# Performance work log

Hardware: AMD Instinct MI355X
Metric: run time of the kernel (lower is better)

Reference implementation:

```python
import jax, jax.numpy as jnp
import numpy as np

# Mamba3TextEncoder config (class .small() defaults)
B_SZ, SEQ = 4, 512
VOCAB, D_MODEL, N_LAYERS = 32000, 768, 12
N_STATE, EXPAND, HEADDIM, NGROUPS, EMBED = 64, 2, 32, 1, 1536
D_INNER = EXPAND * D_MODEL            # 1536
NHEADS = D_INNER // HEADDIM           # 48
CONV_DIM = D_INNER + 2 * NGROUPS * N_STATE  # 1664 (x, B, C go through depthwise conv)
K_CONV = 4
PROJ_IN = 2 * D_INNER + 2 * NGROUPS * N_STATE + NHEADS  # z, xBC, dt


def setup_inputs() -> dict:
    key = jax.random.key(0)
    ks = jax.random.split(key, 16)
    s = 0.02
    return {
        "token_ids": jax.random.randint(ks[0], (B_SZ, SEQ), 0, VOCAB),
        "embed_W": jax.random.normal(ks[1], (VOCAB, D_MODEL), jnp.float32) * s,
        "ln_W": jnp.ones((N_LAYERS, D_MODEL), jnp.float32),
        "in_proj_W": jax.random.normal(ks[2], (N_LAYERS, D_MODEL, PROJ_IN), jnp.float32) * s,
        "conv_W": jax.random.normal(ks[3], (N_LAYERS, CONV_DIM, 1, K_CONV), jnp.float32) * 0.1,
        "conv_b": jnp.zeros((N_LAYERS, CONV_DIM), jnp.float32),
        "dt_bias": jax.random.uniform(ks[4], (N_LAYERS, NHEADS), jnp.float32, -4.6, -2.0),
        "A_log": jnp.tile(jnp.log(jnp.arange(1, NHEADS + 1, dtype=jnp.float32))[None], (N_LAYERS, 1)),
        "D": jnp.ones((N_LAYERS, NHEADS), jnp.float32),
        "norm_W": jnp.ones((N_LAYERS, D_INNER), jnp.float32),
        "out_proj_W": jax.random.normal(ks[5], (N_LAYERS, D_INNER, D_MODEL), jnp.float32) * s,
        "final_norm_W": jnp.ones((D_MODEL,), jnp.float32),
        "proj_W": jax.random.normal(ks[6], (D_MODEL, EMBED), jnp.float32) * s,
        "proj_b": jnp.zeros((EMBED,), jnp.float32),
    }


def _rmsnorm(x, w, eps=1e-5):
    return x * jax.lax.rsqrt(jnp.mean(x * x, axis=-1, keepdims=True) + eps) * w


def _causal_conv(x, w, b):
    # x: [B,S,C] depthwise causal conv, kernel K_CONV
    y = jax.lax.conv_general_dilated(
        x.transpose(0, 2, 1), w, (1,), [(K_CONV - 1, 0)],
        dimension_numbers=("NCH", "OIH", "NCH"), feature_group_count=CONV_DIM)
    return y.transpose(0, 2, 1) + b


def _ssm(xs, dt, A, Bm, Cm):
    # selective scan. xs:[B,S,H,P] dt:[B,S,H] A:[H] Bm,Cm:[B,S,N] (ngroups=1)
    decay = jnp.exp(dt * A)              # [B,S,H]
    dtx = dt[..., None] * xs             # [B,S,H,P]
    h0 = jnp.zeros((xs.shape[0], NHEADS, HEADDIM, N_STATE), xs.dtype)

    def step(h, inp):
        dec, dx, b, c = inp              # [B,H],[B,H,P],[B,N],[B,N]
        h = dec[..., None, None] * h + dx[..., None] * b[:, None, None, :]
        y = jnp.einsum("bhpn,bn->bhp", h, c)
        return h, y

    inputs = (decay.transpose(1, 0, 2), dtx.transpose(1, 0, 2, 3),
              Bm.transpose(1, 0, 2), Cm.transpose(1, 0, 2))
    _, ys = jax.lax.scan(step, h0, inputs)
    return ys.transpose(1, 0, 2, 3)      # [B,S,H,P]


def reference(token_ids, embed_W, ln_W, in_proj_W, conv_W, conv_b, dt_bias,
              A_log, D, norm_W, out_proj_W, final_norm_W, proj_W, proj_b):
    x = embed_W[token_ids]                               # [B,S,D]
    for l in range(N_LAYERS):
        h = _rmsnorm(x, ln_W[l])
        zxbcdt = h @ in_proj_W[l]                        # [B,S,PROJ_IN]
        z = zxbcdt[..., :D_INNER]
        xBC = zxbcdt[..., D_INNER:D_INNER + CONV_DIM]
        dt_raw = zxbcdt[..., D_INNER + CONV_DIM:]        # [B,S,H]
        xBC = jax.nn.silu(_causal_conv(xBC, conv_W[l], conv_b[l]))
        xs = xBC[..., :D_INNER].reshape(*xBC.shape[:2], NHEADS, HEADDIM)
        Bm = xBC[..., D_INNER:D_INNER + N_STATE]
        Cm = xBC[..., D_INNER + N_STATE:]
        dt = jax.nn.softplus(dt_raw + dt_bias[l])
        A = -jnp.exp(A_log[l])
        y = _ssm(xs, dt, A, Bm, Cm) + D[l][None, None, :, None] * xs
        y = y.reshape(*y.shape[:2], D_INNER)
        y = _rmsnorm(y * jax.nn.silu(z), norm_W[l])      # gated RMSNorm
        x = x + y @ out_proj_W[l]
    x = _rmsnorm(x, final_norm_W)
    pooled = x.mean(axis=1)                              # [B,D]
    proj = pooled @ proj_W + proj_b                      # [B,EMBED]
    n = jnp.sqrt(jnp.sum(proj * proj, axis=-1, keepdims=True))
    return proj / jnp.maximum(n, 1e-12)
```

## Files before the change

kernel.cpp:

```cpp
#include <hip/hip_runtime.h>
#include <math.h>

typedef __bf16 bf16x8 __attribute__((ext_vector_type(8)));
typedef short  s16x8  __attribute__((ext_vector_type(8)));
typedef float  f32x4  __attribute__((ext_vector_type(4)));

static constexpr int BSZ = 4, SEQ = 512, DM = 768;
static constexpr int DIN = 1536, NH = 48, HP = 32, NS = 64;
static constexpr int CDIM = 1664;
static constexpr int PROJ_IN = 3248;
static constexpr int LDZX = 3328;
static constexpr int ROWS = BSZ * SEQ;
static constexpr int EMBED = 1536;
static constexpr int NLAYERS = 12;

using gptr_t = const __attribute__((address_space(1))) void*;
using lptr_t = __attribute__((address_space(3))) void*;

__device__ __forceinline__ unsigned short f2bf(float f) {
  unsigned u = __builtin_bit_cast(unsigned, f);
  u += 0x7FFF + ((u >> 16) & 1);
  return (unsigned short)(u >> 16);
}
__device__ __forceinline__ float bf2f(unsigned short u) {
  unsigned v = (unsigned)u << 16;
  return __builtin_bit_cast(float, v);
}
__device__ __forceinline__ float sigm(float x) { return 1.f / (1.f + __expf(-x)); }
__device__ __forceinline__ float sp(float x) { return (x > 15.f) ? x : log1pf(__expf(x)); }

__device__ __forceinline__ void gll16(const void* g, void* l) {
  __builtin_amdgcn_global_load_lds((gptr_t)g, (lptr_t)l, 16, 0, 0);
}
__device__ __forceinline__ f32x4 mfma16(s16x8 a, s16x8 b, f32x4 c) {
  return __builtin_amdgcn_mfma_f32_16x16x32_bf16(
      __builtin_bit_cast(bf16x8, a), __builtin_bit_cast(bf16x8, b), c, 0, 0, 0);
}

template <int NW>
__device__ __forceinline__ float block_sum(float v) {
#pragma unroll
  for (int o = 32; o; o >>= 1) v += __shfl_xor(v, o);
  __shared__ float red[NW];
  if ((threadIdx.x & 63) == 0) red[threadIdx.x >> 6] = v;
  __syncthreads();
  float s = red[0];
#pragma unroll
  for (int i = 1; i < NW; ++i) s += red[i];
  return s;
}

__global__ void embed_k(const int* __restrict__ tok, const float* __restrict__ eW,
                        float* __restrict__ x, unsigned short* __restrict__ x16,
                        float* __restrict__ ssq1p) {
  int bt = blockIdx.x, tid = threadIdx.x;
  float4 v = ((const float4*)(eW + (size_t)tok[bt] * DM))[tid];
  ((float4*)(x + (size_t)bt * DM))[tid] = v;
  unsigned long long pk =
      (unsigned long long)f2bf(v.x) | ((unsigned long long)f2bf(v.y) << 16) |
      ((unsigned long long)f2bf(v.z) << 32) | ((unsigned long long)f2bf(v.w) << 48);
  *(unsigned long long*)(x16 + (size_t)bt * DM + tid * 4) = pk;
  float ss = v.x * v.x + v.y * v.y + v.z * v.z + v.w * v.w;
  float tot = block_sum<3>(ss);
  if (tid < 24) ssq1p[(size_t)bt * 24 + tid] = (tid == 0) ? tot : 0.f;
}

__global__ void transpose_cvt(const float* __restrict__ W, const float* __restrict__ sc,
                              unsigned short* __restrict__ Wt, int K, int N, int Npad) {
  __shared__ float tile[32][68];
  int l = blockIdx.z;
  const float* Wl = W + (size_t)l * K * N;
  const float* scl = sc + (size_t)l * K;
  unsigned short* Wtl = Wt + (size_t)l * Npad * K;
  int nb = blockIdx.x * 64, kb = blockIdx.y * 32;
  int tid = threadIdx.x;
#pragma unroll
  for (int rep = 0; rep < 2; ++rep) {
    int f = rep * 256 + tid;
    int k = f >> 4, c4 = f & 15;
    int n = nb + c4 * 4;
    float s = scl[kb + k];
    float4 v = {0.f, 0.f, 0.f, 0.f};
    if (n + 3 < N) {
      v = *(const float4*)(Wl + (size_t)(kb + k) * N + n);
    } else if (n < N) {
      float t_[4] = {0.f, 0.f, 0.f, 0.f};
      for (int j = 0; j < 4; ++j) if (n + j < N) t_[j] = Wl[(size_t)(kb + k) * N + n + j];
      v = {t_[0], t_[1], t_[2], t_[3]};
    }
    tile[k][c4 * 4 + 0] = v.x * s; tile[k][c4 * 4 + 1] = v.y * s;
    tile[k][c4 * 4 + 2] = v.z * s; tile[k][c4 * 4 + 3] = v.w * s;
  }
  __syncthreads();
#pragma unroll
  for (int rep = 0; rep < 2; ++rep) {
    int f = rep * 256 + tid;
    int n = f >> 3, k8 = f & 7;
    unsigned long long pk =
        (unsigned long long)f2bf(tile[k8 * 4 + 0][n]) |
        ((unsigned long long)f2bf(tile[k8 * 4 + 1][n]) << 16) |
        ((unsigned long long)f2bf(tile[k8 * 4 + 2][n]) << 32) |
        ((unsigned long long)f2bf(tile[k8 * 4 + 3][n]) << 48);
    *(unsigned long long*)(Wtl + (size_t)(nb + n) * K + kb + k8 * 4) = pk;
  }
}

template <int BM, int BN, int MODE>
__global__ __launch_bounds__(256) void gemm_k(
    const unsigned short* __restrict__ A, const unsigned short* __restrict__ Bt,
    int K, const float* __restrict__ ssqp, void* __restrict__ O0,
    void* __restrict__ O1, void* __restrict__ O2,
    unsigned short* __restrict__ x16o, float* __restrict__ ssqo) {
  constexpr int AIT = BM / 32, BIT = BN / 32, NST = AIT + BIT;
  constexpr int FM = BM / 32, FN = BN / 32;
  constexpr int NSSQ = (MODE == 0) ? 24 : 48;
  constexpr float INVD = (MODE == 0) ? (1.f / 768.f) : (1.f / 1536.f);
  __shared__ unsigned short lA[2][BM * 64], lB[2][BN * 64];
  __shared__ float rss[BM];
  int tid = threadIdx.x, lane = tid & 63, wv = tid >> 6;
  int flat = blockIdx.y * gridDim.x + blockIdx.x;
  int q8 = (gridDim.x * gridDim.y) >> 3;
  int nf = (flat & 7) * q8 + (flat >> 3);
  int bx = nf % gridDim.x, by = nf / gridDim.x;
  int m0 = by * BM, n0 = bx * BN;
  int wm = (wv >> 1) * (BM / 2), wn = (wv & 1) * (BN / 2);
  int NK = K >> 6;
  auto stage = [&](int kt, int buf) {
#pragma unroll
    for (int i = 0; i < AIT; ++i) {
      int flt = i * 256 + tid, rr = flt >> 3, cc = flt & 7;
      gll16(A + (size_t)(m0 + rr) * K + kt + (cc ^ (rr & 7)) * 8, (char*)lA[buf] + flt * 16);
    }
#pragma unroll
    for (int i = 0; i < BIT; ++i) {
      int flt = i * 256 + tid, rr = flt >> 3, cc = flt & 7;
      gll16(Bt + (size_t)(n0 + rr) * K + kt + (cc ^ (rr & 7)) * 8, (char*)lB[buf] + flt * 16);
    }
  };
  stage(0, 0);
  if (tid < BM) {
    const float* p = ssqp + (size_t)(m0 + tid) * NSSQ;
    float s = 0.f;
#pragma unroll
    for (int j = 0; j < NSSQ; ++j) s += p[j];
    rss[tid] = rsqrtf(s * INVD + 1e-5f);
  }
  __syncthreads();
  f32x4 acc[FM][FN] = {};
  for (int i = 0; i < NK; ++i) {
    if (i + 1 < NK) {
      stage((i + 1) << 6, (i + 1) & 1);
      asm volatile("s_waitcnt vmcnt(%0)" :: "i"(NST) : "memory");
    } else {
      asm volatile("s_waitcnt vmcnt(0)" ::: "memory");
    }
    __builtin_amdgcn_s_barrier();
    __builtin_amdgcn_sched_barrier(0);
    const unsigned short* cA = lA[i & 1];
    const unsigned short* cB = lB[i & 1];
#pragma unroll
    for (int ks = 0; ks < 2; ++ks) {
      s16x8 a[FM], b[FN];
#pragma unroll
      for (int mi = 0; mi < FM; ++mi) {
        int row = wm + mi * 16 + (lane & 15);
        int ch = (ks * 4 + (lane >> 4)) ^ (row & 7);
        a[mi] = *(const s16x8*)((const char*)cA + row * 128 + ch * 16);
      }
#pragma unroll
      for (int nj = 0; nj < FN; ++nj) {
        int row = wn + nj * 16 + (lane & 15);
        int ch = (ks * 4 + (lane >> 4)) ^ (row & 7);
        b[nj] = *(const s16x8*)((const char*)cB + row * 128 + ch * 16);
      }
#pragma unroll
      for (int mi = 0; mi < FM; ++mi)
#pragma unroll
        for (int nj = 0; nj < FN; ++nj)
          acc[mi][nj] = mfma16(a[mi], b[nj], acc[mi][nj]);
    }
    __builtin_amdgcn_s_barrier();
  }
#pragma unroll
  for (int mi = 0; mi < FM; ++mi) {
    int rl0 = wm + mi * 16 + ((lane >> 4) << 2);
    float rsr[4];
#pragma unroll
    for (int rg = 0; rg < 4; ++rg) rsr[rg] = rss[rl0 + rg];
    float part[4] = {0.f, 0.f, 0.f, 0.f};
#pragma unroll
    for (int nj = 0; nj < FN; ++nj) {
      int col = n0 + wn + nj * 16 + (lane & 15);
#pragma unroll
      for (int rg = 0; rg < 4; ++rg) {
        int row = m0 + rl0 + rg;
        float vv = acc[mi][nj][rg] * rsr[rg];
        if constexpr (MODE == 0) {
          if (n0 < DIN) {
            ((unsigned short*)O0)[(size_t)row * DIN + col] = f2bf(vv);
          } else if (n0 < DIN + CDIM) {
            ((float*)O1)[(size_t)row * CDIM + (col - DIN)] = vv;
          } else {
            int c2 = col - (DIN + CDIM);
            if (c2 < NH) ((float*)O2)[(size_t)row * NH + c2] = vv;
          }
        } else {
          size_t idx = (size_t)row * DM + col;
          float xn = vv + ((float*)O0)[idx];
          ((float*)O0)[idx] = xn;
          x16o[idx] = f2bf(xn);
          part[rg] += xn * xn;
        }
      }
    }
    if constexpr (MODE == 1) {
#pragma unroll
      for (int rg = 0; rg < 4; ++rg) {
#pragma unroll
        for (int off = 1; off < 16; off <<= 1) part[rg] += __shfl_xor(part[rg], off);
      }
      if ((lane & 15) == 0) {
#pragma unroll
        for (int rg = 0; rg < 4; ++rg)
          ssqo[(size_t)(m0 + rl0 + rg) * 24 + bx * 2 + (wn >> 5)] = part[rg];
      }
    }
  }
}

__global__ __launch_bounds__(256) void conv_dt_k(
    const float* __restrict__ xbc, const float* __restrict__ cw, const float* __restrict__ cb,
    const float* __restrict__ dtraw, const float* __restrict__ dbias,
    unsigned short* __restrict__ xs16, unsigned short* __restrict__ dtxT,
    unsigned short* __restrict__ Bbf, unsigned short* __restrict__ Cbf,
    float* __restrict__ dts) {
  __shared__ float stg[11][256];
  __shared__ float dtl[8][48];
  int tid = threadIdx.x;
  int chunk = blockIdx.x;
  int bt0 = blockIdx.y * 8;
  int t0 = bt0 & (SEQ - 1);
  int cbase = chunk * 256;
  for (int f = tid; f < 11 * 64; f += 256) {
    int row = f >> 6, c4 = f & 63;
    int s = t0 - 3 + row;
    int col = cbase + c4 * 4;
    float4 v = {0.f, 0.f, 0.f, 0.f};
    if (s >= 0 && col + 3 < CDIM) {
      v = *(const float4*)(xbc + (size_t)(bt0 - 3 + row) * CDIM + col);
    }
    *(float4*)&stg[row][c4 * 4] = v;
  }
  if (chunk < 6) {
    for (int idx = tid; idx < 384; idx += 256) {
      int r = idx / 48, hh = idx - r * 48;
      dtl[r][hh] = sp(dtraw[(size_t)(bt0 + r) * NH + hh] + dbias[hh]);
    }
  }
  __syncthreads();
  int c = cbase + tid;
  if (chunk < 6) {
    float w0 = cw[c * 4], w1 = cw[c * 4 + 1], w2 = cw[c * 4 + 2], w3 = cw[c * 4 + 3];
    float bias = cb[c];
    int hh = c >> 5, p = c & 31, b = bt0 >> 9;
    s16x8 pk;
#pragma unroll
    for (int r = 0; r < 8; ++r) {
      float a = bias + stg[r][tid] * w0 + stg[r + 1][tid] * w1 + stg[r + 2][tid] * w2 +
                stg[r + 3][tid] * w3;
      float sv = a * sigm(a);
      xs16[(size_t)(bt0 + r) * DIN + c] = f2bf(sv);
      pk[r] = (short)f2bf(sv * dtl[r][hh]);
    }
    *reinterpret_cast<s16x8*>(dtxT + ((((size_t)b * NH + hh) * HP + p) * SEQ + t0)) = pk;
  } else if (tid < 128) {
    int cc = DIN + tid;
    float w0 = cw[cc * 4], w1 = cw[cc * 4 + 1], w2 = cw[cc * 4 + 2], w3 = cw[cc * 4 + 3];
    float bias = cb[cc];
#pragma unroll
    for (int r = 0; r < 8; ++r) {
      float a = bias + stg[r][tid] * w0 + stg[r + 1][tid] * w1 + stg[r + 2][tid] * w2 +
                stg[r + 3][tid] * w3;
      float sv = a * sigm(a);
      if (tid < 64) Bbf[(size_t)(bt0 + r) * NS + tid] = f2bf(sv);
      else          Cbf[(size_t)(bt0 + r) * NS + (tid - 64)] = f2bf(sv);
    }
  } else if (tid < 176) {
    int hh = tid - 128;
    float bias_ = dbias[hh];
    float v[8];
#pragma unroll
    for (int r = 0; r < 8; ++r) v[r] = sp(dtraw[(size_t)(bt0 + r) * NH + hh] + bias_);
    float4 a4 = {v[0], v[1], v[2], v[3]}, b4 = {v[4], v[5], v[6], v[7]};
    float* dp = dts + ((size_t)(bt0 >> 9) * NH + hh) * SEQ + t0;
    *(float4*)dp = a4;
    *(float4*)(dp + 4) = b4;
  }
}

__global__ __launch_bounds__(256) void scan_k(
    const unsigned short* __restrict__ Bbf, const unsigned short* __restrict__ Cbf,
    const unsigned short* __restrict__ dtxT, const unsigned short* __restrict__ xs16,
    const float* __restrict__ dts, const unsigned short* __restrict__ zb,
    const float* __restrict__ alog, const float* __restrict__ Dvec,
    unsigned short* __restrict__ g16, float* __restrict__ ssq2p) {
  __shared__ unsigned short CbPt[64 * 64];
  __shared__ unsigned short Bb[2][64 * 64], Dx[2][32 * 64];
  __shared__ float lsb[SEQ];
  __shared__ float wtot[4];
  __shared__ int sfirst;
  int tid = threadIdx.x, lane = tid & 63, wv = tid >> 6;
  int tb = blockIdx.x, h = blockIdx.y, b = blockIdx.z;
  int t0 = tb * 64;
  const unsigned short* dxrow = dtxT + ((size_t)b * NH + h) * HP * SEQ;

#pragma unroll
  for (int i = 0; i < 2; ++i) {
    int flt = i * 256 + tid, rr = flt >> 3, cc = flt & 7;
    gll16(Cbf + (size_t)(b * SEQ + t0 + rr) * NS + (cc ^ (rr & 7)) * 8, (char*)CbPt + flt * 16);
  }
  float Ah = -__expf(alog[h]);
  int t2 = tid * 2;
  float2 dv = *(const float2*)(dts + ((size_t)b * NH + h) * SEQ + t2);
  float d0 = dv.x * Ah, d1 = dv.y * Ah;
  float ps = d0 + d1;
  float v = ps;
#pragma unroll
  for (int off = 1; off < 64; off <<= 1) {
    float u = __shfl_up(v, off);
    if (lane >= off) v += u;
  }
  if (lane == 63) wtot[wv] = v;
  if (tid == 0) sfirst = tb;
  __syncthreads();
  float wpre = 0.f;
#pragma unroll
  for (int w = 0; w < 3; ++w) wpre += (w < wv) ? wtot[w] : 0.f;
  float excl = v + wpre - ps;
  lsb[t2] = excl + d0;
  lsb[t2 + 1] = excl + d0 + d1;
  __syncthreads();
  float REF = lsb[t0];
  if (tid < tb && (REF - lsb[tid * 64 + 63] >= -12.f)) atomicMin(&sfirst, tid);
  __syncthreads();
  int st0 = sfirst;

#pragma unroll
  for (int i = 0; i < 2; ++i) {
    int flt = i * 256 + tid, rr = flt >> 3, cc = flt & 7;
    gll16(Bbf + (size_t)(b * SEQ + st0 * 64 + rr) * NS + (cc ^ (rr & 7)) * 8,
          (char*)Bb[st0 & 1] + flt * 16);
  }
  { int rr = tid >> 3, cc = tid & 7;
    gll16(dxrow + (size_t)rr * SEQ + st0 * 64 + (cc ^ (rr & 7)) * 8,
          (char*)Dx[st0 & 1] + tid * 16); }

  float lt[4], elt[4];
  int trb = wv * 16 + ((lane >> 4) << 2);
#pragma unroll
  for (int rg = 0; rg < 4; ++rg) {
    lt[rg] = lsb[t0 + trb + rg];
    elt[rg] = __expf(lt[rg] - REF);
  }
  s16x8 aC[2];
  f32x4 yacc[2] = {};

  for (int st = st0; st <= tb; ++st) {
    int s0 = st * 64;
    if (st < tb) {
      int s1 = s0 + 64;
#pragma unroll
      for (int i = 0; i < 2; ++i) {
        int flt = i * 256 + tid, rr = flt >> 3, cc = flt & 7;
        gll16(Bbf + (size_t)(b * SEQ + s1 + rr) * NS + (cc ^ (rr & 7)) * 8,
              (char*)Bb[(st + 1) & 1] + flt * 16);
      }
      { int rr = tid >> 3, cc = tid & 7;
        gll16(dxrow + (size_t)rr * SEQ + s1 + (cc ^ (rr & 7)) * 8,
              (char*)Dx[(st + 1) & 1] + tid * 16); }
      asm volatile("s_waitcnt vmcnt(3)" ::: "memory");
    } else {
      asm volatile("s_waitcnt vmcnt(0)" ::: "memory");
    }
    __builtin_amdgcn_s_barrier();
    __builtin_amdgcn_sched_barrier(0);
    const unsigned short* Bcur = Bb[st & 1];
    const unsigned short* Dcur = Dx[st & 1];
    if (st == st0) {
#pragma unroll
      for (int ks = 0; ks < 2; ++ks) {
        int row = wv * 16 + (lane & 15);
        int ch = (ks * 4 + (lane >> 4)) ^ (row & 7);
        aC[ks] = *(const s16x8*)((const char*)CbPt + row * 128 + ch * 16);
      }
    }
    float lsv[4];
#pragma unroll
    for (int sq = 0; sq < 4; ++sq) lsv[sq] = lsb[s0 + sq * 16 + (lane & 15)];
    f32x4 gf[4] = {};
    __builtin_amdgcn_s_setprio(1);
#pragma unroll
    for (int sq = 0; sq < 4; ++sq)
#pragma unroll
      for (int ks = 0; ks < 2; ++ks) {
        int row = sq * 16 + (lane & 15);
        int ch = (ks * 4 + (lane >> 4)) ^ (row & 7);
        s16x8 bB = *(const s16x8*)((const char*)Bcur + row * 128 + ch * 16);
        gf[sq] = mfma16(aC[ks], bB, gf[sq]);
      }
    __builtin_amdgcn_s_setprio(0);
    if (st < tb) {
      float es[4];
#pragma unroll
      for (int sq = 0; sq < 4; ++sq) es[sq] = __expf(REF - lsv[sq]);
#pragma unroll
      for (int sq = 0; sq < 4; ++sq) {
        int scol = sq * 16 + (lane & 15);
#pragma unroll
        for (int rg = 0; rg < 4; ++rg) {
          int trow = trb + rg;
          int off = (trow * 128 + scol * 2) ^ ((trow & 7) << 4);
          *(unsigned short*)((char*)CbPt + off) = f2bf(gf[sq][rg] * (elt[rg] * es[sq]));
        }
      }
    } else {
#pragma unroll
      for (int sq = 0; sq < 4; ++sq) {
        int scol = sq * 16 + (lane & 15);
        int sg = s0 + scol;
#pragma unroll
        for (int rg = 0; rg < 4; ++rg) {
          int trow = trb + rg, tg = t0 + trow;
          float wgt = (sg <= tg) ? __expf(lt[rg] - lsv[sq]) : 0.f;
          int off = (trow * 128 + scol * 2) ^ ((trow & 7) << 4);
          *(unsigned short*)((char*)CbPt + off) = f2bf(gf[sq][rg] * wgt);
        }
      }
    }
    __builtin_amdgcn_s_setprio(1);
#pragma unroll
    for (int ks = 0; ks < 2; ++ks) {
      int row = wv * 16 + (lane & 15);
      int ch = (ks * 4 + (lane >> 4)) ^ (row & 7);
      s16x8 aP = *(const s16x8*)((const char*)CbPt + row * 128 + ch * 16);
#pragma unroll
      for (int pq = 0; pq < 2; ++pq) {
        int prow = pq * 16 + (lane & 15);
        int pch = (ks * 4 + (lane >> 4)) ^ (prow & 7);
        s16x8 bD = *(const s16x8*)((const char*)Dcur + prow * 128 + pch * 16);
        yacc[pq] = mfma16(aP, bD, yacc[pq]);
      }
    }
    __builtin_amdgcn_s_setprio(0);
    __builtin_amdgcn_s_barrier();
  }
  float Dh = Dvec[h];
  float part[4] = {0.f, 0.f, 0.f, 0.f};
#pragma unroll
  for (int pq = 0; pq < 2; ++pq) {
#pragma unroll
    for (int rg = 0; rg < 4; ++rg) {
      int trow = trb + rg;
      int tg = t0 + trow;
      int p = pq * 16 + (lane & 15);
      size_t gi = (size_t)(b * SEQ + tg) * DIN + h * HP + p;
      float xv = bf2f(xs16[gi]);
      float yv = yacc[pq][rg] + Dh * xv;
      float zf = bf2f(zb[gi]);
      float g = yv * zf * sigm(zf);
      g16[gi] = f2bf(g);
      part[rg] += g * g;
    }
  }
#pragma unroll
  for (int rg = 0; rg < 4; ++rg) {
#pragma unroll
    for (int off = 1; off < 16; off <<= 1) part[rg] += __shfl_xor(part[rg], off);
  }
  if ((lane & 15) == 0) {
#pragma unroll
    for (int rg = 0; rg < 4; ++rg)
      ssq2p[(size_t)(b * SEQ + t0 + trb + rg) * 48 + h] = part[rg];
  }
}

__global__ void pool_part_k(const float* __restrict__ x, const float* __restrict__ ssq1p,
                            float* __restrict__ pp) {
  __shared__ float rsl[64];
  int b = blockIdx.y, tc = blockIdx.z, d0 = blockIdx.x * 256, tid = threadIdx.x;
  int t0 = tc * 64;
  if (tid < 64) {
    const float* p = ssq1p + (size_t)(b * SEQ + t0 + tid) * 24;
    float s = 0.f;
#pragma unroll
    for (int j = 0; j < 24; ++j) s += p[j];
    rsl[tid] = rsqrtf(s * (1.f / DM) + 1e-5f);
  }
  __syncthreads();
  int d = d0 + tid;
  float s = 0.f;
#pragma unroll 4
  for (int i = 0; i < 64; ++i) s += x[(size_t)(b * SEQ + t0 + i) * DM + d] * rsl[i];
  pp[((size_t)b * 8 + tc) * DM + d] = s;
}
__global__ void proj_k(const float* __restrict__ pp, const float* __restrict__ fnW,
                       const float* __restrict__ pW, const float* __restrict__ pb,
                       float* __restrict__ ptmp) {
  __shared__ float pl[DM];
  __shared__ float red[4][64];
  int e0 = blockIdx.x * 64, b = blockIdx.y, tid = threadIdx.x;
  for (int i = tid; i < DM; i += 256) {
    float s = 0.f;
#pragma unroll
    for (int c = 0; c < 8; ++c) s += pp[((size_t)b * 8 + c) * DM + i];
    pl[i] = s * (1.f / SEQ) * fnW[i];
  }
  __syncthreads();
  int el = tid & 63, g = tid >> 6;
  int e = e0 + el;
  float s = 0.f;
  for (int d = g * 192; d < (g + 1) * 192; ++d)
    s += pl[d] * pW[(size_t)d * EMBED + e];
  red[g][el] = s;
  __syncthreads();
  if (g == 0) ptmp[b * EMBED + e] = red[0][el] + red[1][el] + red[2][el] + red[3][el] + pb[e];
}
__global__ void l2_k(const float* __restrict__ ptmp, float* __restrict__ out) {
  int b = blockIdx.x;
  float v[6], ss = 0.f;
#pragma unroll
  for (int i = 0; i < 6; ++i) {
    v[i] = ptmp[(size_t)b * EMBED + threadIdx.x + i * 256];
    ss += v[i] * v[i];
  }
  float tot = block_sum<4>(ss);
  float inv = 1.f / fmaxf(sqrtf(tot), 1e-12f);
#pragma unroll
  for (int i = 0; i < 6; ++i)
    out[(size_t)b * EMBED + threadIdx.x + i * 256] = v[i] * inv;
}

extern "C" void kernel_launch(void* const* d_in, const int* in_sizes, int n_in,
                              void* d_out, int out_size, void* d_ws, size_t ws_size,
                              hipStream_t stream) {
  const int*   tok  = (const int*)d_in[0];
  const float* embW = (const float*)d_in[1];
  const float* lnW  = (const float*)d_in[2];
  const float* ipW  = (const float*)d_in[3];
  const float* cW   = (const float*)d_in[4];
  const float* cB   = (const float*)d_in[5];
  const float* dtB  = (const float*)d_in[6];
  const float* Alog = (const float*)d_in[7];
  const float* Dv   = (const float*)d_in[8];
  const float* nW   = (const float*)d_in[9];
  const float* opW  = (const float*)d_in[10];
  const float* fnW  = (const float*)d_in[11];
  const float* pW   = (const float*)d_in[12];
  const float* pb   = (const float*)d_in[13];
  float* out = (float*)d_out;

  char* wsp = (char*)d_ws;
  auto alloc = [&](size_t bytes) {
    char* p = wsp;
    wsp += (bytes + 255) & ~(size_t)255;
    return p;
  };
  float* x      = (float*)alloc((size_t)ROWS * DM * 4);
  float* xbc    = (float*)alloc((size_t)ROWS * CDIM * 4);
  float* dtraw  = (float*)alloc((size_t)ROWS * NH * 4);
  float* dts    = (float*)alloc((size_t)BSZ * NH * SEQ * 4);
  float* ssq1p  = (float*)alloc((size_t)ROWS * 24 * 4);
  float* ssq2p  = (float*)alloc((size_t)ROWS * 48 * 4);
  float* pp     = (float*)alloc((size_t)BSZ * 8 * DM * 4);
  float* ptmp   = (float*)alloc((size_t)BSZ * EMBED * 4);
  unsigned short* x16   = (unsigned short*)alloc((size_t)ROWS * DM * 2);
  unsigned short* zb    = (unsigned short*)alloc((size_t)ROWS * DIN * 2);
  unsigned short* xs16  = (unsigned short*)alloc((size_t)ROWS * DIN * 2);
  unsigned short* g16   = (unsigned short*)alloc((size_t)ROWS * DIN * 2);
  unsigned short* dtxT  = (unsigned short*)alloc((size_t)BSZ * NH * HP * SEQ * 2);
  unsigned short* Bbf   = (unsigned short*)alloc((size_t)ROWS * NS * 2);
  unsigned short* Cbf   = (unsigned short*)alloc((size_t)ROWS * NS * 2);
  unsigned short* wtA   = (unsigned short*)alloc((size_t)NLAYERS * LDZX * DM * 2);
  unsigned short* wtO   = (unsigned short*)alloc((size_t)NLAYERS * DM * DIN * 2);

  embed_k<<<ROWS, 192, 0, stream>>>(tok, embW, x, x16, ssq1p);
  transpose_cvt<<<dim3(LDZX / 64, DM / 32, NLAYERS), 256, 0, stream>>>(
      ipW, lnW, wtA, DM, PROJ_IN, LDZX);
  transpose_cvt<<<dim3(DM / 64, DIN / 32, NLAYERS), 256, 0, stream>>>(
      opW, nW, wtO, DIN, DM, DM);

  for (int l = 0; l < NLAYERS; ++l) {
    gemm_k<128, 64, 0><<<dim3(LDZX / 64, ROWS / 128), 256, 0, stream>>>(
        x16, wtA + (size_t)l * LDZX * DM, DM, ssq1p, zb, xbc, dtraw, nullptr, nullptr);
    conv_dt_k<<<dim3(7, ROWS / 8), 256, 0, stream>>>(
        xbc, cW + (size_t)l * CDIM * 4, cB + (size_t)l * CDIM, dtraw, dtB + l * NH,
        xs16, dtxT, Bbf, Cbf, dts);
    scan_k<<<dim3(SEQ / 64, NH, BSZ), 256, 0, stream>>>(
        Bbf, Cbf, dtxT, xs16, dts, zb, Alog + l * NH, Dv + l * NH, g16, ssq2p);
    gemm_k<64, 64, 1><<<dim3(DM / 64, ROWS / 64), 256, 0, stream>>>(
        g16, wtO + (size_t)l * DM * DIN, DIN, ssq2p, x, nullptr, nullptr, x16, ssq1p);
  }

  pool_part_k<<<dim3(DM / 256, BSZ, 8), 256, 0, stream>>>(x, ssq1p, pp);
  proj_k<<<dim3(EMBED / 64, BSZ), 256, 0, stream>>>(pp, fnW, pW, pb, ptmp);
  l2_k<<<BSZ, 256, 0, stream>>>(ptmp, out);
}
```

Before: 921.9 us.

## Process 128-row output tiles per scan block with 512 threads

The chunked scan kernel now has each block handle 128 time steps (8 waves) instead of 64, so each B and dt·x source chunk loaded into shared memory feeds two 64-row output tiles. The grid halves along the sequence axis and the prefix-sum of decay is computed with one element per thread. The aim is to cut redundant global loads and per-block setup, at the cost of fewer blocks, more LDS per block, and per-wave waitcnt handling. The diagonal masking now covers the last two source chunks for all rows, which lets the upper tile use masked weights even on the earlier chunk.

```diff
diff --git a/kernel.cpp b/kernel.cpp
--- a/kernel.cpp
+++ b/kernel.cpp
@@ -298,87 +298,83 @@
   }
 }
 
-__global__ __launch_bounds__(256) void scan_k(
+__global__ __launch_bounds__(512) void scan_k(
     const unsigned short* __restrict__ Bbf, const unsigned short* __restrict__ Cbf,
     const unsigned short* __restrict__ dtxT, const unsigned short* __restrict__ xs16,
     const float* __restrict__ dts, const unsigned short* __restrict__ zb,
     const float* __restrict__ alog, const float* __restrict__ Dvec,
     unsigned short* __restrict__ g16, float* __restrict__ ssq2p) {
-  __shared__ unsigned short CbPt[64 * 64];
+  __shared__ unsigned short CbPt[128 * 64];
   __shared__ unsigned short Bb[2][64 * 64], Dx[2][32 * 64];
   __shared__ float lsb[SEQ];
-  __shared__ float wtot[4];
+  __shared__ float wtot[8];
   __shared__ int sfirst;
   int tid = threadIdx.x, lane = tid & 63, wv = tid >> 6;
-  int tb = blockIdx.x, h = blockIdx.y, b = blockIdx.z;
-  int t0 = tb * 64;
+  int tb2 = blockIdx.x;
+  int h = blockIdx.y, b = blockIdx.z;
+  int T0 = tb2 * 128;
+  int ST_LAST = 2 * tb2 + 1;
   const unsigned short* dxrow = dtxT + ((size_t)b * NH + h) * HP * SEQ;
 
 #pragma unroll
   for (int i = 0; i < 2; ++i) {
-    int flt = i * 256 + tid, rr = flt >> 3, cc = flt & 7;
-    gll16(Cbf + (size_t)(b * SEQ + t0 + rr) * NS + (cc ^ (rr & 7)) * 8, (char*)CbPt + flt * 16);
+    int flt = i * 512 + tid, rr = flt >> 3, cc = flt & 7;
+    gll16(Cbf + (size_t)(b * SEQ + T0 + rr) * NS + (cc ^ (rr & 7)) * 8, (char*)CbPt + flt * 16);
   }
   float Ah = -__expf(alog[h]);
-  int t2 = tid * 2;
-  float2 dv = *(const float2*)(dts + ((size_t)b * NH + h) * SEQ + t2);
-  float d0 = dv.x * Ah, d1 = dv.y * Ah;
-  float ps = d0 + d1;
-  float v = ps;
+  float d = dts[((size_t)b * NH + h) * SEQ + tid] * Ah;
+  float v = d;
 #pragma unroll
   for (int off = 1; off < 64; off <<= 1) {
     float u = __shfl_up(v, off);
     if (lane >= off) v += u;
   }
   if (lane == 63) wtot[wv] = v;
-  if (tid == 0) sfirst = tb;
+  if (tid == 0) sfirst = 2 * tb2;
   __syncthreads();
   float wpre = 0.f;
 #pragma unroll
-  for (int w = 0; w < 3; ++w) wpre += (w < wv) ? wtot[w] : 0.f;
-  float excl = v + wpre - ps;
-  lsb[t2] = excl + d0;
-  lsb[t2 + 1] = excl + d0 + d1;
-  __syncthreads();
-  float REF = lsb[t0];
-  if (tid < tb && (REF - lsb[tid * 64 + 63] >= -12.f)) atomicMin(&sfirst, tid);
+  for (int w = 0; w < 7; ++w) wpre += (w < wv) ? wtot[w] : 0.f;
+  lsb[tid] = v + wpre;
+  __syncthreads();
+  float REF = lsb[T0];
+  if (tid < 2 * tb2 && (REF - lsb[tid * 64 + 63] >= -12.f)) atomicMin(&sfirst, tid);
   __syncthreads();
   int st0 = sfirst;
 
-#pragma unroll
-  for (int i = 0; i < 2; ++i) {
-    int flt = i * 256 + tid, rr = flt >> 3, cc = flt & 7;
+  { int rr = tid >> 3, cc = tid & 7;
     gll16(Bbf + (size_t)(b * SEQ + st0 * 64 + rr) * NS + (cc ^ (rr & 7)) * 8,
-          (char*)Bb[st0 & 1] + flt * 16);
-  }
-  { int rr = tid >> 3, cc = tid & 7;
+          (char*)Bb[st0 & 1] + tid * 16); }
+  if (tid < 256) {
+    int rr = tid >> 3, cc = tid & 7;
     gll16(dxrow + (size_t)rr * SEQ + st0 * 64 + (cc ^ (rr & 7)) * 8,
-          (char*)Dx[st0 & 1] + tid * 16); }
+          (char*)Dx[st0 & 1] + tid * 16);
+  }
 
   float lt[4], elt[4];
   int trb = wv * 16 + ((lane >> 4) << 2);
 #pragma unroll
   for (int rg = 0; rg < 4; ++rg) {
-    lt[rg] = lsb[t0 + trb + rg];
+    lt[rg] = lsb[T0 + trb + rg];
     elt[rg] = __expf(lt[rg] - REF);
   }
   s16x8 aC[2];
   f32x4 yacc[2] = {};
 
-  for (int st = st0; st <= tb; ++st) {
+  for (int st = st0; st <= ST_LAST; ++st) {
     int s0 = st * 64;
-    if (st < tb) {
+    if (st < ST_LAST) {
       int s1 = s0 + 64;
-#pragma unroll
-      for (int i = 0; i < 2; ++i) {
-        int flt = i * 256 + tid, rr = flt >> 3, cc = flt & 7;
+      { int rr = tid >> 3, cc = tid & 7;
         gll16(Bbf + (size_t)(b * SEQ + s1 + rr) * NS + (cc ^ (rr & 7)) * 8,
-              (char*)Bb[(st + 1) & 1] + flt * 16);
-      }
-      { int rr = tid >> 3, cc = tid & 7;
+              (char*)Bb[(st + 1) & 1] + tid * 16); }
+      if (tid < 256) {
+        int rr = tid >> 3, cc = tid & 7;
         gll16(dxrow + (size_t)rr * SEQ + s1 + (cc ^ (rr & 7)) * 8,
-              (char*)Dx[(st + 1) & 1] + tid * 16); }
-      asm volatile("s_waitcnt vmcnt(3)" ::: "memory");
+              (char*)Dx[(st + 1) & 1] + tid * 16);
+      }
+      if (wv < 4) { asm volatile("s_waitcnt vmcnt(2)" ::: "memory"); }
+      else        { asm volatile("s_waitcnt vmcnt(1)" ::: "memory"); }
     } else {
       asm volatile("s_waitcnt vmcnt(0)" ::: "memory");
     }
@@ -409,7 +405,7 @@
         gf[sq] = mfma16(aC[ks], bB, gf[sq]);
       }
     __builtin_amdgcn_s_setprio(0);
-    if (st < tb) {
+    if (st < ST_LAST - 1) {
       float es[4];
 #pragma unroll
       for (int sq = 0; sq < 4; ++sq) es[sq] = __expf(REF - lsv[sq]);
@@ -430,7 +426,7 @@
         int sg = s0 + scol;
 #pragma unroll
         for (int rg = 0; rg < 4; ++rg) {
-          int trow = trb + rg, tg = t0 + trow;
+          int trow = trb + rg, tg = T0 + trow;
           float wgt = (sg <= tg) ? __expf(lt[rg] - lsv[sq]) : 0.f;
           int off = (trow * 128 + scol * 2) ^ ((trow & 7) << 4);
           *(unsigned short*)((char*)CbPt + off) = f2bf(gf[sq][rg] * wgt);
@@ -461,7 +457,7 @@
 #pragma unroll
     for (int rg = 0; rg < 4; ++rg) {
       int trow = trb + rg;
-      int tg = t0 + trow;
+      int tg = T0 + trow;
       int p = pq * 16 + (lane & 15);
       size_t gi = (size_t)(b * SEQ + tg) * DIN + h * HP + p;
       float xv = bf2f(xs16[gi]);
@@ -480,7 +476,7 @@
   if ((lane & 15) == 0) {
 #pragma unroll
     for (int rg = 0; rg < 4; ++rg)
-      ssq2p[(size_t)(b * SEQ + t0 + trb + rg) * 48 + h] = part[rg];
+      ssq2p[(size_t)(b * SEQ + T0 + trb + rg) * 48 + h] = part[rg];
   }
 }
 
@@ -595,7 +591,7 @@
     conv_dt_k<<<dim3(7, ROWS / 8), 256, 0, stream>>>(
         xbc, cW + (size_t)l * CDIM * 4, cB + (size_t)l * CDIM, dtraw, dtB + l * NH,
         xs16, dtxT, Bbf, Cbf, dts);
-    scan_k<<<dim3(SEQ / 64, NH, BSZ), 256, 0, stream>>>(
+    scan_k<<<dim3(SEQ / 128, NH, BSZ), 512, 0, stream>>>(
         Bbf, Cbf, dtxT, xs16, dts, zb, Alog + l * NH, Dv + l * NH, g16, ssq2p);
     gemm_k<64, 64, 1><<<dim3(DM / 64, ROWS / 64), 256, 0, stream>>>(
         g16, wtO + (size_t)l * DM * DIN, DIN, ssq2p, x, nullptr, nullptr, x16, ssq1p);
```

Measured after the change: 970.9 us. +5.3%, slower.
